# Optimization experiments

Measured on AMD Instinct MI355X. Metric: run time of the kernel, lower is better.

The kernel has to match this reference:

```python
import jax, jax.numpy as jnp
import numpy as np

EPS = 1e-5
P = 3  # p_size
BW = 1.0  # bandwidth


def _instance_norm(x):
    # calc_mean_std: per (B,C) mean/std over spatial dims, unbiased var (torch default)
    b, c, h, w = x.shape
    flat = x.reshape(b, c, h * w)
    mean = flat.mean(-1)[:, :, None, None]
    std = jnp.sqrt(flat.var(-1, ddof=1) + EPS)[:, :, None, None]
    return (x - mean) / std


def _conv1x1(x, w, bias):
    # x: (B,C,H,W), w: (O,C), bias: (O,)
    return jnp.einsum('oc,bchw->bohw', w, x) + bias[None, :, None, None]


def _patches_scaled(x, scale):
    # ReflectionPad2d(1) + Unfold(3) -> (B, HW, C*9), torch layout (c slow, k fast),
    # with ContextAtten scale applied over the 9 kernel positions.
    b, c, h, w = x.shape
    pad = jnp.pad(x, ((0, 0), (0, 0), (1, 1), (1, 1)), mode='reflect')
    # (B,C,H,W,9)
    p9 = jnp.stack([pad[:, :, di:di + h, dj:dj + w]
                    for di in range(P) for dj in range(P)], axis=-1)
    p9 = p9 * scale  # broadcast over last (kernel) axis
    # -> (B,H,W,C,9) -> (B, HW, C*9)
    return p9.transpose(0, 2, 3, 1, 4).reshape(b, h * w, c * P * P)


def setup_inputs() -> dict:
    key = jax.random.key(0)
    ks = jax.random.split(key, 12)
    B, C, H, W = 2, 512, 64, 64
    IC = 256
    f32 = jnp.float32
    inp = {
        'content': jax.random.normal(ks[0], (B, C, H, W), f32),
        'style': jax.random.normal(ks[1], (B, C, H, W), f32),
        'fusion_style': jax.random.normal(ks[2], (B, C, H, W), f32),
        'theta_w': jax.random.normal(ks[3], (IC, C), f32) * np.sqrt(2.0 / C),
        'theta_b': jnp.zeros((IC,), f32),
        'phi_w': jax.random.normal(ks[4], (IC, C), f32) * np.sqrt(2.0 / C),
        'phi_b': jnp.zeros((IC,), f32),
        'g_w': jax.random.normal(ks[5], (IC, C), f32) * np.sqrt(2.0 / C),
        'g_b': jnp.zeros((IC,), f32),
        'W_w': jax.random.normal(ks[6], (C, IC), f32) * np.sqrt(2.0 / IC),
        'W_b': jnp.zeros((C,), f32),
        'scale': jnp.ones((P * P,), f32),
    }
    return inp


def reference(content, style, fusion_style, theta_w, theta_b, phi_w, phi_b,
              g_w, g_b, W_w, W_b, scale):
    B, C, H, W = content.shape
    IC = theta_w.shape[0]
    HW = H * W

    # g on fusion_style -> (B, HW, IC)
    g_s = _conv1x1(fusion_style, g_w, g_b).reshape(B, IC, HW).transpose(0, 2, 1)

    # instance-normalize content/style (normal=True path)
    xn = _instance_norm(content)
    sn = _instance_norm(style)

    theta_x = _conv1x1(xn, theta_w, theta_b)
    phi_s = _conv1x1(sn, phi_w, phi_b)

    theta_p = _patches_scaled(theta_x, scale)  # (B, HW, IC*9)
    phi_p = _patches_scaled(phi_s, scale)      # (B, HW, IC*9)

    f = jnp.einsum('blk,bmk->blm', theta_p, phi_p) * BW  # (B, HW, HW)
    f_div_C = jax.nn.softmax(f, axis=-1)

    y = jnp.einsum('blm,bmo->blo', f_div_C, g_s)  # (B, HW, IC)
    y = y.transpose(0, 2, 1).reshape(B, IC, H, W)
    W_y = _conv1x1(y, W_w, W_b)  # (B, C, H, W)
    # isTraining=True path: conf_map = 0
    return W_y
```

## Files before the change

### kernel.cpp

```cpp
#include <hip/hip_runtime.h>
#include <stdint.h>

typedef __attribute__((ext_vector_type(8))) __bf16 bf16x8;
typedef __attribute__((ext_vector_type(4))) float f32x4;
typedef __attribute__((ext_vector_type(4))) unsigned int uint4v;

__device__ __forceinline__ float bf2f(unsigned short u){
  unsigned int x = ((unsigned int)u) << 16;
  return __builtin_bit_cast(float, x);
}
__device__ __forceinline__ unsigned short f2bf(float f){
  unsigned int x = __builtin_bit_cast(unsigned int, f);
  x += 0x7FFFu + ((x >> 16) & 1u);
  return (unsigned short)(x >> 16);
}

#define OUT_PART 4
#define OUT_PARTH 5

template<int OM>
__global__ __launch_bounds__(256)
void gemm_bt(const unsigned short* __restrict__ A, int lda,
             const unsigned short* __restrict__ Bt, int ldb,
             int kchunk, void* __restrict__ Out, int ldo,
             size_t zStride, size_t aBatch, size_t bBatch,
             int sMask, int sShift)
{
  __shared__ uint4v AsmBuf[1024];
  __shared__ uint4v BsmBuf[1024];
  char* Asm = (char*)AsmBuf;
  char* Bsm = (char*)BsmBuf;

  const int tid  = threadIdx.x;
  const int lane = tid & 63;
  const int wave = tid >> 6;
  const int wy = wave >> 1, wx = wave & 1;
  const int lm = lane & 15, quad = lane >> 4;
  const int tileM = blockIdx.y * 128;
  const int tileN = blockIdx.x * 128;
  const int z = blockIdx.z;
  const int slice = z & sMask;
  const int batch = z >> sShift;

  A  += (size_t)slice*kchunk + (size_t)batch*aBatch;
  Bt += (size_t)slice*kchunk + (size_t)batch*bBatch;

  const int sr0 = tid >> 2, sc0 = tid & 3;
  const int sr1 = sr0 + 64;
  const size_t gA0 = (size_t)(tileM + sr0)*lda + ((sc0 ^ ((sr0 >> 1) & 3)) << 3);
  const size_t gA1 = (size_t)(tileM + sr1)*lda + ((sc0 ^ ((sr1 >> 1) & 3)) << 3);
  const size_t gB0 = (size_t)(tileN + sr0)*ldb + ((sc0 ^ ((sr0 >> 1) & 3)) << 3);
  const size_t gB1 = (size_t)(tileN + sr1)*ldb + ((sc0 ^ ((sr1 >> 1) & 3)) << 3);
  const int lOff0 = sr0*64 + sc0*16;
  const int lOff1 = sr1*64 + sc0*16;

  int aOff[4], bOff[4];
#pragma unroll
  for (int t = 0; t < 4; ++t){
    int ra = wy*64 + t*16 + lm;
    aOff[t] = ra*64 + ((quad ^ ((ra >> 1) & 3)) << 4);
    int rb = wx*64 + t*16 + lm;
    bOff[t] = rb*64 + ((quad ^ ((rb >> 1) & 3)) << 4);
  }

  f32x4 acc[4][4] = {};

  const int ksteps = kchunk >> 5;
  uint4v a0v = *(const uint4v*)(A + gA0);
  uint4v a1v = *(const uint4v*)(A + gA1);
  uint4v b0v = *(const uint4v*)(Bt + gB0);
  uint4v b1v = *(const uint4v*)(Bt + gB1);

  for (int kt = 0; kt < ksteps; ++kt){
    char* As = Asm + (kt & 1)*8192;
    char* Bs = Bsm + (kt & 1)*8192;
    *(uint4v*)(As + lOff0) = a0v;
    *(uint4v*)(As + lOff1) = a1v;
    *(uint4v*)(Bs + lOff0) = b0v;
    *(uint4v*)(Bs + lOff1) = b1v;
    __syncthreads();
    if (kt + 1 < ksteps){
      const unsigned short* Ak = A + (kt + 1)*32;
      const unsigned short* Bk = Bt + (kt + 1)*32;
      a0v = *(const uint4v*)(Ak + gA0);
      a1v = *(const uint4v*)(Ak + gA1);
      b0v = *(const uint4v*)(Bk + gB0);
      b1v = *(const uint4v*)(Bk + gB1);
    }
    bf16x8 af[4], bfr[4];
#pragma unroll
    for (int t = 0; t < 4; ++t){
      af[t]  = __builtin_bit_cast(bf16x8, *(const uint4v*)(As + aOff[t]));
      bfr[t] = __builtin_bit_cast(bf16x8, *(const uint4v*)(Bs + bOff[t]));
    }
#pragma unroll
    for (int tm = 0; tm < 4; ++tm)
#pragma unroll
      for (int tn = 0; tn < 4; ++tn)
        acc[tm][tn] = __builtin_amdgcn_mfma_f32_16x16x32_bf16(af[tm], bfr[tn], acc[tm][tn], 0, 0, 0);
  }

#pragma unroll
  for (int tm = 0; tm < 4; ++tm){
    const int rowb = tileM + wy*64 + tm*16 + quad*4;
#pragma unroll
    for (int tn = 0; tn < 4; ++tn){
      const int col = tileN + wx*64 + tn*16 + lm;
#pragma unroll
      for (int r = 0; r < 4; ++r){
        const float v = acc[tm][tn][r];
        const size_t idx = (size_t)z*zStride + (size_t)(rowb + r)*ldo + col;
        if (OM == OUT_PART) ((float*)Out)[idx] = v;
        else                ((unsigned short*)Out)[idx] = f2bf(v);
      }
    }
  }
}

template<int OM>
__global__ __launch_bounds__(256)
void gemm_wide(const unsigned short* __restrict__ A, int lda,
               const unsigned short* __restrict__ Bt, int ldb,
               int kchunk, void* __restrict__ Out, int ldo,
               size_t zStride, size_t aBatch, size_t bBatch,
               int sMask, int sShift)
{
  __shared__ uint4v AsmBuf[1024];
  __shared__ uint4v BsmBuf[2048];
  char* Asm = (char*)AsmBuf;
  char* Bsm = (char*)BsmBuf;

  const int tid  = threadIdx.x;
  const int lane = tid & 63;
  const int wave = tid >> 6;
  const int wy = wave >> 1, wx = wave & 1;
  const int lm = lane & 15, quad = lane >> 4;
  const int tileM = blockIdx.y * 128;
  const int tileN = blockIdx.x * 256;
  const int z = blockIdx.z;
  const int slice = z & sMask;
  const int batch = z >> sShift;

  A  += (size_t)slice*kchunk + (size_t)batch*aBatch;
  Bt += (size_t)slice*kchunk + (size_t)batch*bBatch;

  const int sr = tid >> 2, sc = tid & 3;
  size_t gA[2]; int lA[2];
  size_t gB[4]; int lB[4];
#pragma unroll
  for (int i = 0; i < 2; ++i){
    const int r = sr + 64*i;
    gA[i] = (size_t)(tileM + r)*lda + ((sc ^ ((r >> 1) & 3)) << 3);
    lA[i] = r*64 + sc*16;
  }
#pragma unroll
  for (int i = 0; i < 4; ++i){
    const int r = sr + 64*i;
    gB[i] = (size_t)(tileN + r)*ldb + ((sc ^ ((r >> 1) & 3)) << 3);
    lB[i] = r*64 + sc*16;
  }

  int aOff[4], bOff[8];
#pragma unroll
  for (int t = 0; t < 4; ++t){
    const int ra = wy*64 + t*16 + lm;
    aOff[t] = ra*64 + ((quad ^ ((ra >> 1) & 3)) << 4);
  }
#pragma unroll
  for (int t = 0; t < 8; ++t){
    const int rb = wx*128 + t*16 + lm;
    bOff[t] = rb*64 + ((quad ^ ((rb >> 1) & 3)) << 4);
  }

  f32x4 acc[4][8] = {};

  const int ksteps = kchunk >> 5;
  uint4v av[2], bv[4];
#pragma unroll
  for (int i = 0; i < 2; ++i) av[i] = *(const uint4v*)(A + gA[i]);
#pragma unroll
  for (int i = 0; i < 4; ++i) bv[i] = *(const uint4v*)(Bt + gB[i]);

  for (int kt = 0; kt < ksteps; ++kt){
    char* As = Asm + (kt & 1)*8192;
    char* Bs = Bsm + (kt & 1)*16384;
#pragma unroll
    for (int i = 0; i < 2; ++i) *(uint4v*)(As + lA[i]) = av[i];
#pragma unroll
    for (int i = 0; i < 4; ++i) *(uint4v*)(Bs + lB[i]) = bv[i];
    __syncthreads();
    if (kt + 1 < ksteps){
      const unsigned short* Ak = A + (kt + 1)*32;
      const unsigned short* Bk = Bt + (kt + 1)*32;
#pragma unroll
      for (int i = 0; i < 2; ++i) av[i] = *(const uint4v*)(Ak + gA[i]);
#pragma unroll
      for (int i = 0; i < 4; ++i) bv[i] = *(const uint4v*)(Bk + gB[i]);
    }
    bf16x8 af[4], bfr[8];
#pragma unroll
    for (int t = 0; t < 4; ++t)
      af[t] = __builtin_bit_cast(bf16x8, *(const uint4v*)(As + aOff[t]));
#pragma unroll
    for (int t = 0; t < 8; ++t)
      bfr[t] = __builtin_bit_cast(bf16x8, *(const uint4v*)(Bs + bOff[t]));
#pragma unroll
    for (int tm = 0; tm < 4; ++tm)
#pragma unroll
      for (int tn = 0; tn < 8; ++tn)
        acc[tm][tn] = __builtin_amdgcn_mfma_f32_16x16x32_bf16(af[tm], bfr[tn], acc[tm][tn], 0, 0, 0);
  }

#pragma unroll
  for (int tm = 0; tm < 4; ++tm){
    const int rowb = tileM + wy*64 + tm*16 + quad*4;
#pragma unroll
    for (int tn = 0; tn < 8; ++tn){
      const int col = tileN + wx*128 + tn*16 + lm;
#pragma unroll
      for (int r = 0; r < 4; ++r){
        const float v = acc[tm][tn][r];
        const size_t idx = (size_t)z*zStride + (size_t)(rowb + r)*ldo + col;
        if (OM == OUT_PART) ((float*)Out)[idx] = v;
        else                ((unsigned short*)Out)[idx] = f2bf(v);
      }
    }
  }
}

__global__ __launch_bounds__(256)
void gemm_big(const unsigned short* __restrict__ A, int lda,
              const unsigned short* __restrict__ Bt, int ldb,
              int K, float* __restrict__ Out, int ldo,
              size_t aBatch, size_t bBatch, size_t oBatch)
{
  __shared__ uint4v AsmBuf[2048];
  char* Asm = (char*)AsmBuf;

  const int tid  = threadIdx.x;
  const int lane = tid & 63;
  const int wave = tid >> 6;
  const int wy = wave >> 1, wx = wave & 1;
  const int lm = lane & 15, quad = lane >> 4;
  const int tileM = blockIdx.y * 256;
  const int tileN = blockIdx.x * 128;
  const int z = blockIdx.z;

  A  += (size_t)z*aBatch;
  Bt += (size_t)z*bBatch;
  Out += (size_t)z*oBatch;

  const int sr = tid >> 2, sc = tid & 3;
  size_t gA[4]; int lA[4];
#pragma unroll
  for (int i = 0; i < 4; ++i){
    const int r = sr + 64*i;
    gA[i] = (size_t)(tileM + r)*lda + ((sc ^ ((r >> 1) & 3)) << 3);
    lA[i] = r*64 + sc*16;
  }

  int aOff[8];
#pragma unroll
  for (int t = 0; t < 8; ++t){
    const int ra = wy*128 + t*16 + lm;
    aOff[t] = ra*64 + ((quad ^ ((ra >> 1) & 3)) << 4);
  }
  size_t gBF[4];
#pragma unroll
  for (int t = 0; t < 4; ++t){
    const int rb = wx*64 + t*16 + lm;
    gBF[t] = (size_t)(tileN + rb)*ldb + quad*8;
  }

  f32x4 acc[8][4] = {};

  const int ksteps = K >> 5;
  uint4v av[4];
#pragma unroll
  for (int i = 0; i < 4; ++i) av[i] = *(const uint4v*)(A + gA[i]);
  bf16x8 bnx[4];
#pragma unroll
  for (int t = 0; t < 4; ++t)
    bnx[t] = __builtin_bit_cast(bf16x8, *(const uint4v*)(Bt + gBF[t]));

  for (int kt = 0; kt < ksteps; ++kt){
    char* As = Asm + (kt & 1)*16384;
#pragma unroll
    for (int i = 0; i < 4; ++i) *(uint4v*)(As + lA[i]) = av[i];
    __syncthreads();
    bf16x8 bcur[4];
#pragma unroll
    for (int t = 0; t < 4; ++t) bcur[t] = bnx[t];
    if (kt + 1 < ksteps){
      const unsigned short* Ak = A + (kt + 1)*32;
      const unsigned short* Bk = Bt + (kt + 1)*32;
#pragma unroll
      for (int i = 0; i < 4; ++i) av[i] = *(const uint4v*)(Ak + gA[i]);
#pragma unroll
      for (int t = 0; t < 4; ++t)
        bnx[t] = __builtin_bit_cast(bf16x8, *(const uint4v*)(Bk + gBF[t]));
    }
    bf16x8 af[8];
#pragma unroll
    for (int t = 0; t < 8; ++t)
      af[t] = __builtin_bit_cast(bf16x8, *(const uint4v*)(As + aOff[t]));
#pragma unroll
    for (int tm = 0; tm < 8; ++tm)
#pragma unroll
      for (int tn = 0; tn < 4; ++tn)
        acc[tm][tn] = __builtin_amdgcn_mfma_f32_16x16x32_bf16(af[tm], bcur[tn], acc[tm][tn], 0, 0, 0);
  }

#pragma unroll
  for (int tm = 0; tm < 8; ++tm){
    const int rowb = tileM + wy*128 + tm*16 + quad*4;
#pragma unroll
    for (int tn = 0; tn < 4; ++tn){
      const int col = tileN + wx*64 + tn*16 + lm;
#pragma unroll
      for (int r = 0; r < 4; ++r)
        Out[(size_t)(rowb + r)*ldo + col] = acc[tm][tn][r];
    }
  }
}

__global__ __launch_bounds__(256)
void reduce_tp(const float* __restrict__ part,
               const float* __restrict__ tb, const float* __restrict__ pb,
               unsigned short* __restrict__ th, unsigned short* __restrict__ ph)
{
  const size_t i = (size_t)blockIdx.x*256 + threadIdx.x;
  const int which = (int)(i >> 21);
  const size_t j = i & 0x1FFFFFu;
  const int col = (int)(j & 255u);
  float v = 0.f;
#pragma unroll
  for (int s = 0; s < 4; ++s)
    v += part[(size_t)((which << 2) + s)*2097152 + j];
  v += (which ? pb : tb)[col];
  unsigned short hi = f2bf(v);
  unsigned short lo = f2bf(v - bf2f(hi));
  const size_t o = (j >> 8)*768 + col;
  unsigned short* O = which ? ph : th;
  const int dup = which ? 512 : 256;
  const int loo = which ? 256 : 512;
  O[o] = hi; O[o + dup] = hi; O[o + loo] = lo;
}

__global__ __launch_bounds__(256)
void reduce_g(const unsigned short* __restrict__ part,
              const float* __restrict__ gb, unsigned short* __restrict__ gs)
{
  const size_t i = (size_t)blockIdx.x*256 + threadIdx.x;
  float v = 0.f;
#pragma unroll
  for (int s = 0; s < 4; ++s) v += bf2f(part[(size_t)s*2097152 + i]);
  gs[i] = f2bf(v + gb[i >> 13]);
}

__global__ __launch_bounds__(256)
void reduce_y(const unsigned short* __restrict__ part,
              unsigned short* __restrict__ yb)
{
  const size_t i = (size_t)blockIdx.x*256 + threadIdx.x;
  const int b = (int)(i >> 20);
  const size_t j = i & 0xFFFFFu;
  float v = 0.f;
#pragma unroll
  for (int s = 0; s < 8; ++s)
    v += bf2f(part[(size_t)((b << 3) + s)*1048576 + j]);
  yb[i] = f2bf(v);
}

__global__ __launch_bounds__(256)
void reduce_w(const float* __restrict__ part, const float* __restrict__ wb,
              void* __restrict__ Out, const unsigned int* __restrict__ flagPtr)
{
  const size_t i = (size_t)blockIdx.x*256 + threadIdx.x;
  const int b = (int)(i >> 21);
  const size_t j = i & 0x1FFFFFu;
  float v = part[(size_t)(b << 1)*2097152 + j]
          + part[(size_t)((b << 1) | 1)*2097152 + j]
          + wb[(i >> 12) & 511u];
  if (flagPtr[0]) ((float*)Out)[i] = v;
  else            ((unsigned short*)Out)[i] = f2bf(v);
}

__global__ __launch_bounds__(256)
void detect_prep(const void* __restrict__ content,
                 const void* tb, const void* pb, const void* gb, const void* wb,
                 const void* sc,
                 unsigned int* __restrict__ flag, float* __restrict__ scale_c,
                 float* tb_c, float* pb_c, float* gb_c, float* wb_c)
{
  __shared__ int cnt;
  __shared__ unsigned int flg;
  const int tid = threadIdx.x;
  if (tid == 0) cnt = 0;
  __syncthreads();
  unsigned int w = ((const unsigned int*)content)[tid];
  int e = (w >> 23) & 0xFF;
  if (e >= 0x70 && e <= 0x8F) atomicAdd(&cnt, 1);
  __syncthreads();
  if (tid == 0){ flg = (cnt >= 128) ? 1u : 0u; flag[0] = flg; }
  __syncthreads();
  const unsigned int f = flg;
  auto rd = [&](const void* p, int i)->float{
    return f ? ((const float*)p)[i] : bf2f(((const unsigned short*)p)[i]);
  };
  if (tid < 9) scale_c[tid] = rd(sc, tid);
  tb_c[tid] = rd(tb, tid);
  pb_c[tid] = rd(pb, tid);
  gb_c[tid] = rd(gb, tid);
  wb_c[tid] = rd(wb, tid);
  wb_c[tid + 256] = rd(wb, tid + 256);
}

__global__ __launch_bounds__(256)
void conv_weights(const void* tw, const void* pw, const void* gw, const void* www,
                  const unsigned int* __restrict__ flagPtr,
                  unsigned short* __restrict__ wdup,
                  unsigned short* __restrict__ gwc,
                  unsigned short* __restrict__ wwc)
{
  const unsigned int fl = flagPtr[0];
  const int sec = blockIdx.y;
  const int idx = blockIdx.x*256 + threadIdx.x;
  auto rd = [&](const void* p, int i)->float{
    return fl ? ((const float*)p)[i] : bf2f(((const unsigned short*)p)[i]);
  };
  if (sec < 2){
    const void* w = sec ? pw : tw;
    const int o = idx >> 9, c = idx & 511;
    float v = rd(w, o*512 + c);
    unsigned short hi = f2bf(v);
    unsigned short lo = f2bf(v - bf2f(hi));
    unsigned short* base = wdup + (size_t)sec*256*1536 + o*1536;
    base[c] = hi; base[512 + c] = lo; base[1024 + c] = hi;
  } else if (sec == 2){
    const int o = idx >> 9, c = idx & 511;
    gwc[o*512 + c] = f2bf(rd(gw, o*512 + c));
  } else {
    const int o = idx >> 8, c = idx & 255;
    wwc[o*256 + c] = f2bf(rd(www, o*256 + c));
  }
}

__global__ __launch_bounds__(256)
void stats_all(const void* __restrict__ content, const void* __restrict__ style,
               const unsigned int* __restrict__ flagPtr,
               float* __restrict__ statsC, float* __restrict__ statsS)
{
  const unsigned int fl = flagPtr[0];
  const void* X = blockIdx.z ? style : content;
  float* stats = blockIdx.z ? statsS : statsC;
  const int bc = blockIdx.x;
  const int tid = threadIdx.x;
  float s = 0.f, q = 0.f;
  if (fl){
    const f32x4* row = (const f32x4*)((const float*)X + (size_t)bc*4096);
#pragma unroll
    for (int i = 0; i < 4; ++i){
      f32x4 v = row[tid + i*256];
#pragma unroll
      for (int j = 0; j < 4; ++j){ s += v[j]; q += v[j]*v[j]; }
    }
  } else {
    const uint4v* row = (const uint4v*)((const unsigned short*)X + (size_t)bc*4096);
#pragma unroll
    for (int i = 0; i < 2; ++i){
      uint4v u = row[tid + i*256];
#pragma unroll
      for (int j = 0; j < 4; ++j){
        float a = bf2f((unsigned short)(u[j] & 0xffffu));
        float b = bf2f((unsigned short)(u[j] >> 16));
        s += a + b; q += a*a + b*b;
      }
    }
  }
#pragma unroll
  for (int off = 32; off > 0; off >>= 1){
    s += __shfl_down(s, off);
    q += __shfl_down(q, off);
  }
  __shared__ float rs[4], rq[4];
  if ((tid & 63) == 0){ rs[tid >> 6] = s; rq[tid >> 6] = q; }
  __syncthreads();
  if (tid == 0){
    s = rs[0] + rs[1] + rs[2] + rs[3];
    q = rq[0] + rq[1] + rq[2] + rq[3];
    float mean = s * (1.0f/4096.0f);
    float var  = (q - 4096.0f*mean*mean) * (1.0f/4095.0f);
    stats[bc*2 + 0] = mean;
    stats[bc*2 + 1] = 1.0f / sqrtf(var + 1e-5f);
  }
}

__global__ __launch_bounds__(256)
void norm_all(const void* __restrict__ content, const void* __restrict__ style,
              const void* __restrict__ fusion,
              const float* __restrict__ statsC, const float* __restrict__ statsS,
              unsigned short* __restrict__ xn, unsigned short* __restrict__ sn,
              unsigned short* __restrict__ fst,
              const unsigned int* __restrict__ flagPtr)
{
  __shared__ float tile[64][65];
  const unsigned int fl = flagPtr[0];
  const int z = blockIdx.z;
  const int which = z >> 1;
  const int b  = z & 1;
  const int l0 = blockIdx.x * 64;
  const int c0 = blockIdx.y * 64;
  const int tid = threadIdx.x;
  const int tx = tid & 63, ty = tid >> 6;

  const void* X = which == 0 ? content : (which == 1 ? style : fusion);
#pragma unroll
  for (int p = 0; p < 16; ++p){
    const int cc = ty + p*4;
    const size_t src = ((size_t)b*512 + c0 + cc)*4096 + l0 + tx;
    tile[cc][tx] = fl ? ((const float*)X)[src]
                      : bf2f(((const unsigned short*)X)[src]);
  }
  __syncthreads();
  if (which < 2){
    const float* stats = which ? statsS : statsC;
    const float mean = stats[(b*512 + c0 + tx)*2 + 0];
    const float inv  = stats[(b*512 + c0 + tx)*2 + 1];
    unsigned short* Out = which ? sn : xn;
#pragma unroll
    for (int p = 0; p < 16; ++p){
      const int lj = ty + p*4;
      const float v = (tile[tx][lj] - mean) * inv;
      const size_t o = ((size_t)b*4096 + l0 + lj)*1536 + c0 + tx;
      const unsigned short hi = f2bf(v);
      Out[o] = hi;
      Out[o + 512] = hi;
      Out[o + 1024] = f2bf(v - bf2f(hi));
    }
  } else {
#pragma unroll
    for (int p = 0; p < 16; ++p){
      const int lj = ty + p*4;
      const size_t o = ((size_t)b*4096 + l0 + lj)*512 + c0 + tx;
      fst[o] = f2bf(tile[tx][lj]);
    }
  }
}

__global__ __launch_bounds__(256)
void softmax_rows(const float* __restrict__ Gbase, const float* __restrict__ scale_c,
                  unsigned short* __restrict__ Pbase)
{
  const int bb = blockIdx.x >> 12;
  const int l  = blockIdx.x & 4095;
  const float* G = Gbase + (size_t)bb*16777216;
  unsigned short* P = Pbase + (size_t)bb*16777216;
  const int yy = l >> 6, xx = l & 63;
  const int tid = threadIdx.x;

  float s2[9];
  const float* rowp[9];
#pragma unroll
  for (int di = 0; di < 3; ++di){
    int ry = yy + di - 1; ry = ry < 0 ? 1 : (ry > 63 ? 62 : ry);
#pragma unroll
    for (int dj = 0; dj < 3; ++dj){
      int rx = xx + dj - 1; rx = rx < 0 ? 1 : (rx > 63 ? 62 : rx);
      const int k = di*3 + dj;
      const float s = scale_c[k];
      s2[k] = s*s;
      rowp[k] = G + (size_t)(ry*64 + rx)*4096;
    }
  }

  float fv[16];
  float mx = -3.0e38f;
#pragma unroll
  for (int i = 0; i < 16; ++i){
    const int m = tid + i*256;
    const int my = m >> 6, mxo = m & 63;
    int cy[3], cx[3];
#pragma unroll
    for (int d = 0; d < 3; ++d){
      int t0 = my + d - 1;  cy[d] = (t0 < 0 ? 1 : (t0 > 63 ? 62 : t0))*64;
      int t1 = mxo + d - 1; cx[d] = (t1 < 0 ? 1 : (t1 > 63 ? 62 : t1));
    }
    float v = 0.f;
#pragma unroll
    for (int di = 0; di < 3; ++di)
#pragma unroll
      for (int dj = 0; dj < 3; ++dj)
        v = fmaf(s2[di*3+dj], rowp[di*3+dj][cy[di] + cx[dj]], v);
    fv[i] = v;
    mx = fmaxf(mx, v);
  }

  __shared__ float redA[4], redB[4];
#pragma unroll
  for (int off = 32; off > 0; off >>= 1) mx = fmaxf(mx, __shfl_down(mx, off));
  if ((tid & 63) == 0) redA[tid >> 6] = mx;
  __syncthreads();
  mx = fmaxf(fmaxf(redA[0], redA[1]), fmaxf(redA[2], redA[3]));

  float sum = 0.f;
#pragma unroll
  for (int i = 0; i < 16; ++i){ fv[i] = __expf(fv[i] - mx); sum += fv[i]; }
#pragma unroll
  for (int off = 32; off > 0; off >>= 1) sum += __shfl_down(sum, off);
  if ((tid & 63) == 0) redB[tid >> 6] = sum;
  __syncthreads();
  sum = redB[0] + redB[1] + redB[2] + redB[3];
  const float inv = 1.0f / sum;

  unsigned short* Prow = P + (size_t)l*4096;
#pragma unroll
  for (int i = 0; i < 16; ++i) Prow[tid + i*256] = f2bf(fv[i]*inv);
}

extern "C" void kernel_launch(void* const* d_in, const int* in_sizes, int n_in,
                              void* d_out, int out_size, void* d_ws, size_t ws_size,
                              hipStream_t stream)
{
  const void* content = d_in[0];
  const void* style   = d_in[1];
  const void* fusion  = d_in[2];
  const void* theta_w = d_in[3];
  const void* theta_b = d_in[4];
  const void* phi_w   = d_in[5];
  const void* phi_b   = d_in[6];
  const void* g_w     = d_in[7];
  const void* g_b     = d_in[8];
  const void* W_w     = d_in[9];
  const void* W_b     = d_in[10];
  const void* scale   = d_in[11];

  char* ws = (char*)d_ws;
  size_t off = 0;
  auto take = [&](size_t bytes)->char*{
    char* p = ws + off; off += (bytes + 255) & ~(size_t)255; return p;
  };

  unsigned int* flag  = (unsigned int*)take(256);
  float* scale_c      = (float*)take(256);
  float* tb_c         = (float*)take(1024);
  float* pb_c         = (float*)take(1024);
  float* gb_c         = (float*)take(1024);
  float* wb_c         = (float*)take(2048);
  float* statsC       = (float*)take(1024ull*2*4);
  float* statsS       = (float*)take(1024ull*2*4);
  unsigned short* wdup = (unsigned short*)take(2ull*256*1536*2);
  unsigned short* gwc  = (unsigned short*)take(256ull*512*2);
  unsigned short* wwc  = (unsigned short*)take(512ull*256*2);
  unsigned short* th   = (unsigned short*)take(8192ull*768*2);
  unsigned short* ph   = (unsigned short*)take(8192ull*768*2);
  unsigned short* gs   = (unsigned short*)take(256ull*8192*2);
  unsigned short* yb   = (unsigned short*)take(2ull*4096*256*2);
  float* G0            = (float*)take(4096ull*4096*4);
  float* G1            = (float*)take(4096ull*4096*4);
  char* unionC         = take(64ull*1024*1024);
  unsigned short* xn   = (unsigned short*)unionC;
  unsigned short* sn   = (unsigned short*)(unionC + 8192ull*1536*2);
  unsigned short* fst  = (unsigned short*)(unionC + 2ull*8192*1536*2);
  unsigned short* P    = (unsigned short*)unionC;

  float* partTP          = G0;
  unsigned short* partG  = (unsigned short*)G1;
  unsigned short* partY  = (unsigned short*)G0;
  float* partW           = G1;

  detect_prep<<<1, 256, 0, stream>>>(content, theta_b, phi_b, g_b, W_b, scale,
                                     flag, scale_c, tb_c, pb_c, gb_c, wb_c);
  conv_weights<<<dim3(512,4), 256, 0, stream>>>(theta_w, phi_w, g_w, W_w, flag,
                                                wdup, gwc, wwc);
  stats_all<<<dim3(1024,1,2), 256, 0, stream>>>(content, style, flag, statsC, statsS);
  norm_all<<<dim3(64,8,6), 256, 0, stream>>>(content, style, fusion,
                                             statsC, statsS, xn, sn, fst, flag);

  gemm_wide<OUT_PART><<<dim3(1,64,8), 256, 0, stream>>>(
      xn, 1536, wdup, 1536, 384, partTP, 256, 8192ull*256,
      8192ull*1536, 256ull*1536, 3, 2);
  reduce_tp<<<16384, 256, 0, stream>>>(partTP, tb_c, pb_c, th, ph);

  gemm_bt<OUT_PARTH><<<dim3(64,2,4), 256, 0, stream>>>(
      gwc, 512, fst, 512, 128, partG, 8192, 256ull*8192, 0, 0, 3, 2);
  reduce_g<<<8192, 256, 0, stream>>>(partG, gb_c, gs);

  gemm_big<<<dim3(32,16,2), 256, 0, stream>>>(
      th, 768, ph, 768, 768, G0, 4096,
      4096ull*768, 4096ull*768, (size_t)(G1 - G0));

  softmax_rows<<<8192, 256, 0, stream>>>(G0, scale_c, P);

  gemm_wide<OUT_PARTH><<<dim3(1,32,16), 256, 0, stream>>>(
      P, 4096, gs, 8192, 512, partY, 256, 4096ull*256,
      16777216ull, 4096ull, 7, 3);
  reduce_y<<<8192, 256, 0, stream>>>(partY, yb);

  gemm_bt<OUT_PART><<<dim3(32,4,4), 256, 0, stream>>>(
      wwc, 256, yb, 256, 128, partW, 4096, 512ull*4096,
      0, 4096ull*256, 1, 1);
  reduce_w<<<16384, 256, 0, stream>>>(partW, wb_c, d_out, flag);
}
```

Before: 393.0 us.

## Rewrite attention-score GEMM with 256x256 tiles and direct global-to-LDS loads

Replaces the 256x128-tile, 4-wave score GEMM with a 256x256-tile, 8-wave kernel. Both A and B now stream through double-buffered LDS using global_load_lds asynchronous copies, replacing register-staged A and direct-from-global B fragments. The kernel adds explicit waitcnt, barriers, sched_barrier and setprio around MFMA phases to overlap the next tile's loads with compute. This is meant to raise data reuse and hide global-load latency, at the cost of 64KB of LDS per block, more barriers, and a smaller grid.

```diff
diff --git a/kernel.cpp b/kernel.cpp
--- a/kernel.cpp
+++ b/kernel.cpp
@@ -228,87 +228,105 @@
   }
 }
 
-__global__ __launch_bounds__(256)
-void gemm_big(const unsigned short* __restrict__ A, int lda,
-              const unsigned short* __restrict__ Bt, int ldb,
-              int K, float* __restrict__ Out, int ldo,
-              size_t aBatch, size_t bBatch, size_t oBatch)
-{
-  __shared__ uint4v AsmBuf[2048];
-  char* Asm = (char*)AsmBuf;
+typedef const __attribute__((address_space(1))) unsigned int* gas1_t;
+typedef __attribute__((address_space(3))) unsigned int* las3_t;
+__device__ __forceinline__ void gload16(const void* g, void* l){
+  __builtin_amdgcn_global_load_lds((gas1_t)g, (las3_t)l, 16, 0, 0);
+}
+
+__global__ __launch_bounds__(512)
+void gemm_big256(const unsigned short* __restrict__ A, int lda,
+                 const unsigned short* __restrict__ Bt, int ldb,
+                 int K, float* __restrict__ Out, int ldo,
+                 size_t aBatch, size_t bBatch, size_t oBatch)
+{
+  __shared__ char lds[65536];
 
   const int tid  = threadIdx.x;
   const int lane = tid & 63;
-  const int wave = tid >> 6;
-  const int wy = wave >> 1, wx = wave & 1;
+  const int wv   = tid >> 6;
+  const int wy = wv >> 2, wx = wv & 3;
   const int lm = lane & 15, quad = lane >> 4;
   const int tileM = blockIdx.y * 256;
-  const int tileN = blockIdx.x * 128;
+  const int tileN = blockIdx.x * 256;
   const int z = blockIdx.z;
 
-  A  += (size_t)z*aBatch;
-  Bt += (size_t)z*bBatch;
+  A   += (size_t)z*aBatch;
+  Bt  += (size_t)z*bBatch;
   Out += (size_t)z*oBatch;
 
-  const int sr = tid >> 2, sc = tid & 3;
-  size_t gA[4]; int lA[4];
-#pragma unroll
-  for (int i = 0; i < 4; ++i){
-    const int r = sr + 64*i;
-    gA[i] = (size_t)(tileM + r)*lda + ((sc ^ ((r >> 1) & 3)) << 3);
-    lA[i] = r*64 + sc*16;
-  }
-
-  int aOff[8];
-#pragma unroll
-  for (int t = 0; t < 8; ++t){
-    const int ra = wy*128 + t*16 + lm;
-    aOff[t] = ra*64 + ((quad ^ ((ra >> 1) & 3)) << 4);
-  }
-  size_t gBF[4];
-#pragma unroll
-  for (int t = 0; t < 4; ++t){
-    const int rb = wx*64 + t*16 + lm;
-    gBF[t] = (size_t)(tileN + rb)*ldb + quad*8;
-  }
+  const int srow  = tid >> 2;
+  const int selem = (((tid & 3) ^ ((tid >> 3) & 3)) << 3);
+  const size_t gAs  = (size_t)(tileM + srow)*lda + selem;
+  const size_t gAs2 = gAs + (size_t)128*lda;
+  const size_t gBs  = (size_t)(tileN + srow)*ldb + selem;
+  const size_t gBs2 = gBs + (size_t)128*ldb;
+  const int ldsSt = tid << 4;
+
+  const int xq    = (quad ^ ((lm >> 1) & 3)) << 4;
+  const int aBase = (wy*128 + lm)*64 + xq;
+  const int bBase = (wx*64  + lm)*64 + xq;
 
   f32x4 acc[8][4] = {};
-
-  const int ksteps = K >> 5;
-  uint4v av[4];
-#pragma unroll
-  for (int i = 0; i < 4; ++i) av[i] = *(const uint4v*)(A + gA[i]);
-  bf16x8 bnx[4];
-#pragma unroll
-  for (int t = 0; t < 4; ++t)
-    bnx[t] = __builtin_bit_cast(bf16x8, *(const uint4v*)(Bt + gBF[t]));
-
-  for (int kt = 0; kt < ksteps; ++kt){
-    char* As = Asm + (kt & 1)*16384;
-#pragma unroll
-    for (int i = 0; i < 4; ++i) *(uint4v*)(As + lA[i]) = av[i];
-    __syncthreads();
-    bf16x8 bcur[4];
-#pragma unroll
-    for (int t = 0; t < 4; ++t) bcur[t] = bnx[t];
-    if (kt + 1 < ksteps){
-      const unsigned short* Ak = A + (kt + 1)*32;
+  const int nk = K >> 5;
+
+  gload16(A  + gAs,  lds + ldsSt);
+  gload16(A  + gAs2, lds + ldsSt + 8192);
+  gload16(Bt + gBs,  lds + 16384 + ldsSt);
+  gload16(Bt + gBs2, lds + 16384 + ldsSt + 8192);
+
+  for (int kt = 0; kt < nk; ++kt){
+    if (kt + 1 < nk){
+      char* nbuf = lds + ((kt + 1) & 1)*32768;
+      const unsigned short* Ak = A  + (kt + 1)*32;
       const unsigned short* Bk = Bt + (kt + 1)*32;
-#pragma unroll
-      for (int i = 0; i < 4; ++i) av[i] = *(const uint4v*)(Ak + gA[i]);
-#pragma unroll
-      for (int t = 0; t < 4; ++t)
-        bnx[t] = __builtin_bit_cast(bf16x8, *(const uint4v*)(Bk + gBF[t]));
-    }
-    bf16x8 af[8];
-#pragma unroll
-    for (int t = 0; t < 8; ++t)
-      af[t] = __builtin_bit_cast(bf16x8, *(const uint4v*)(As + aOff[t]));
-#pragma unroll
-    for (int tm = 0; tm < 8; ++tm)
-#pragma unroll
-      for (int tn = 0; tn < 4; ++tn)
-        acc[tm][tn] = __builtin_amdgcn_mfma_f32_16x16x32_bf16(af[tm], bcur[tn], acc[tm][tn], 0, 0, 0);
+      gload16(Ak + gAs,  nbuf + ldsSt);
+      gload16(Ak + gAs2, nbuf + ldsSt + 8192);
+      gload16(Bk + gBs,  nbuf + 16384 + ldsSt);
+      gload16(Bk + gBs2, nbuf + 16384 + ldsSt + 8192);
+      asm volatile("s_waitcnt vmcnt(4)" ::: "memory");
+    } else {
+      asm volatile("s_waitcnt vmcnt(0)" ::: "memory");
+    }
+    __builtin_amdgcn_s_barrier();
+    __builtin_amdgcn_sched_barrier(0);
+
+    const char* As = lds + (kt & 1)*32768;
+    const char* Bs = As + 16384;
+
+    bf16x8 a[4], b[4];
+#pragma unroll
+    for (int n = 0; n < 4; ++n)
+      b[n] = __builtin_bit_cast(bf16x8, *(const uint4v*)(Bs + bBase + n*1024));
+#pragma unroll
+    for (int m = 0; m < 4; ++m)
+      a[m] = __builtin_bit_cast(bf16x8, *(const uint4v*)(As + aBase + m*1024));
+
+    __builtin_amdgcn_s_barrier();
+    __builtin_amdgcn_s_setprio(1);
+#pragma unroll
+    for (int m = 0; m < 4; ++m)
+#pragma unroll
+      for (int n = 0; n < 4; ++n)
+        acc[m][n] = __builtin_amdgcn_mfma_f32_16x16x32_bf16(a[m], b[n], acc[m][n], 0, 0, 0);
+    __builtin_amdgcn_s_setprio(0);
+    __builtin_amdgcn_s_barrier();
+    __builtin_amdgcn_sched_barrier(0);
+
+#pragma unroll
+    for (int m = 0; m < 4; ++m)
+      a[m] = __builtin_bit_cast(bf16x8, *(const uint4v*)(As + aBase + (m + 4)*1024));
+    __builtin_amdgcn_s_setprio(1);
+#pragma unroll
+    for (int m = 0; m < 4; ++m)
+#pragma unroll
+      for (int n = 0; n < 4; ++n)
+        acc[m + 4][n] = __builtin_amdgcn_mfma_f32_16x16x32_bf16(a[m], b[n], acc[m + 4][n], 0, 0, 0);
+    __builtin_amdgcn_s_setprio(0);
+    __builtin_amdgcn_sched_barrier(0);
+    __builtin_amdgcn_s_barrier();
+    __builtin_amdgcn_sched_barrier(0);
+    asm volatile("" ::: "memory");
   }
 
 #pragma unroll
@@ -686,7 +704,7 @@
       gwc, 512, fst, 512, 128, partG, 8192, 256ull*8192, 0, 0, 3, 2);
   reduce_g<<<8192, 256, 0, stream>>>(partG, gb_c, gs);
 
-  gemm_big<<<dim3(32,16,2), 256, 0, stream>>>(
+  gemm_big256<<<dim3(16,16,2), 512, 0, stream>>>(
       th, 768, ph, 768, 768, G0, 4096,
       4096ull*768, 4096ull*768, (size_t)(G1 - G0));
 
```

Result: faster. 383.2 us (-2.5%).
